# Kernel tuning notes

Measured on AMD Instinct MI355X. Metric: run time of the kernel, lower is better.

Reference implementation:

```python
import jax, jax.numpy as jnp
import numpy as np

E, N, HID, NH = 250000, 50000, 128, 4
HD = HID // NH  # head_dim = 32


def setup_inputs() -> dict:
    key = jax.random.key(0)
    ks = jax.random.split(key, 16)
    f = lambda k, s: jax.random.normal(k, s, dtype=jnp.float32)
    w = lambda k, s: jax.random.normal(k, s, dtype=jnp.float32) * 0.05
    return {
        "edge_attr": f(ks[0], (E, HID)),
        "node_features": f(ks[1], (N, HID)),
        "regime_probs": jax.random.uniform(ks[2], (3,), dtype=jnp.float32),
        # phase_query / phase_key: Linear(hidden+3 -> hidden)
        "Wq": w(ks[3], (HID, HID + 3)), "bq": jnp.zeros((HID,), jnp.float32),
        "Wk": w(ks[4], (HID, HID + 3)), "bk": jnp.zeros((HID,), jnp.float32),
        # phase_value: Linear(hidden -> hidden)
        "Wv": w(ks[5], (HID, HID)), "bv": jnp.zeros((HID,), jnp.float32),
        # nn.MultiheadAttention packed in-projection [3*hid, hid] and out_proj
        "W_in": w(ks[6], (3 * HID, HID)), "b_in": jnp.zeros((3 * HID,), jnp.float32),
        "W_mo": w(ks[7], (HID, HID)), "b_mo": jnp.zeros((HID,), jnp.float32),
        # output_proj
        "Wo": w(ks[8], (HID, HID)), "bo": jnp.zeros((HID,), jnp.float32),
        "edge_index": jax.random.randint(ks[9], (2, E), 0, N, dtype=jnp.int64),
    }


def reference(edge_attr, node_features, regime_probs,
              Wq, bq, Wk, bk, Wv, bv,
              W_in, b_in, W_mo, b_mo, Wo, bo,
              edge_index):
    e = edge_attr.shape[0]
    src = node_features[edge_index[0]]  # [E, HID] gather
    tgt = node_features[edge_index[1]]  # [E, HID] gather
    reg = jnp.broadcast_to(regime_probs, (e, regime_probs.shape[0]))  # [E, 3]

    q = jnp.concatenate([src, reg], axis=1) @ Wq.T + bq  # [E, HID]
    k = jnp.concatenate([tgt, reg], axis=1) @ Wk.T + bk  # [E, HID]
    v = edge_attr @ Wv.T + bv                             # [E, HID]

    # nn.MultiheadAttention with seq_len 1 (batch_first): in-proj, heads, softmax, out-proj
    Wiq, Wik, Wiv = jnp.split(W_in, 3, axis=0)
    biq, bik, biv = jnp.split(b_in, 3)
    q2 = (q @ Wiq.T + biq).reshape(e, NH, HD)
    k2 = (k @ Wik.T + bik).reshape(e, NH, HD)
    v2 = (v @ Wiv.T + biv).reshape(e, NH, HD)

    scale = 1.0 / jnp.sqrt(jnp.float32(HD))
    scores = jnp.sum(q2 * k2, axis=-1, keepdims=True) * scale  # [E, NH, 1]
    probs = jax.nn.softmax(scores, axis=-1)                    # seq-len-1 -> all ones
    att = (probs * v2).reshape(e, HID)                         # == v2 merged
    att = att @ W_mo.T + b_mo                                  # MHA out_proj

    out = att @ Wo.T + bo                                      # output_proj
    return edge_attr + 0.5 * out
```

## Files before the change

kernel.cpp:

```cpp
#include <hip/hip_runtime.h>
#include <hip/hip_bf16.h>

#define HID 128

typedef __attribute__((ext_vector_type(8))) short short8;
typedef __attribute__((ext_vector_type(4))) float f32x4;

static __device__ __forceinline__ short f2bf(float x) {
    __hip_bfloat16 h = __float2bfloat16(x);
    return *reinterpret_cast<short*>(&h);
}

__global__ void prep_products(const float* __restrict__ Wo,
                              const float* __restrict__ W_mo,
                              const float* __restrict__ Wiv,
                              const float* __restrict__ Wv,
                              const float* __restrict__ bv,
                              const float* __restrict__ biv,
                              const float* __restrict__ b_mo,
                              const float* __restrict__ bo,
                              float* __restrict__ Pl,
                              float* __restrict__ Pr,
                              float* __restrict__ cv)
{
    const int j = threadIdx.x;
    const int b = blockIdx.x;
    __shared__ float sh[HID];

    if (b < 256) {
        const float* A = (b < 128) ? Wo   : Wiv;
        const float* B = (b < 128) ? W_mo : Wv;
        float*       C = (b < 128) ? Pl   : Pr;
        const int i = b & 127;
        sh[j] = A[i * HID + j];
        __syncthreads();
        float s = 0.f;
        #pragma unroll 16
        for (int k = 0; k < HID; ++k) s += sh[k] * B[k * HID + j];
        C[i * HID + j] = s;
    } else {
        sh[j] = bv[j];
        __syncthreads();
        float t = biv[j];
        #pragma unroll 16
        for (int k = 0; k < HID; ++k) t += Wiv[j * HID + k] * sh[k];
        __syncthreads(); sh[j] = t; __syncthreads();
        t = b_mo[j];
        #pragma unroll 16
        for (int k = 0; k < HID; ++k) t += W_mo[j * HID + k] * sh[k];
        __syncthreads(); sh[j] = t; __syncthreads();
        t = bo[j];
        #pragma unroll 16
        for (int k = 0; k < HID; ++k) t += Wo[j * HID + k] * sh[k];
        cv[j] = 0.5f * t;
    }
}

__global__ void prep_final(const float* __restrict__ Pl,
                           const float* __restrict__ Pr,
                           __hip_bfloat16* __restrict__ Mb)
{
    const int i = blockIdx.x, j = threadIdx.x;
    __shared__ float sh[HID];
    sh[j] = Pl[i * HID + j];
    __syncthreads();
    float s = 0.f;
    #pragma unroll 16
    for (int k = 0; k < HID; ++k) s += sh[k] * Pr[k * HID + j];
    Mb[i * HID + j] = __float2bfloat16(((i == j) ? 1.0f : 0.0f) + 0.5f * s);
}

__global__ __launch_bounds__(256) void edge_gemm(
    const float* __restrict__ ea,
    const __hip_bfloat16* __restrict__ Mb,
    const float* __restrict__ cvec,
    float* __restrict__ out,
    int E, int numTiles)
{
    __shared__ __align__(16) float lds[2][2048];

    const int lane  = threadIdx.x & 63;
    const int wv    = threadIdx.x >> 6;
    const int q     = lane >> 4;
    const int c     = lane & 15;
    const int ncol0 = wv * 32;

    short8 Mfrag[2][4];
    #pragma unroll
    for (int nt = 0; nt < 2; ++nt) {
        const __hip_bfloat16* mp = Mb + (size_t)(ncol0 + nt * 16 + c) * HID + q * 8;
        #pragma unroll
        for (int kk = 0; kk < 4; ++kk)
            Mfrag[nt][kk] = *reinterpret_cast<const short8*>(mp + kk * 32);
    }
    f32x4 cvp[2];
    #pragma unroll
    for (int nt = 0; nt < 2; ++nt)
        cvp[nt] = *reinterpret_cast<const f32x4*>(cvec + ncol0 + nt * 16 + q * 4);

    int t = blockIdx.x;
    if (t >= numTiles) return;
    const int G = gridDim.x;

    const int ldrow = threadIdx.x >> 4;
    const int ldoff = (threadIdx.x & 15) * 32;
    const int wsw  = (ldrow & 7) << 4;
    const int wad0 = ldrow * 512 + (ldoff ^ wsw);
    const int wad1 = wad0 ^ 16;

    const int swz   = (c & 7) << 4;
    const int rbase = c * 512 + ((q * 32) ^ (swz & 0x60));
    const int hx    = swz & 16;

    auto load_tile = [&](int tt, float4& r0, float4& r1) {
        int row = tt * 16 + ldrow; if (row > E - 1) row = E - 1;
        const char* p = (const char*)ea + (size_t)row * 512 + ldoff;
        r0 = *reinterpret_cast<const float4*>(p);
        r1 = *reinterpret_cast<const float4*>(p + 16);
    };
    auto write_tile = [&](int buf, const float4& r0, const float4& r1) {
        char* lb = (char*)&lds[buf][0];
        *reinterpret_cast<float4*>(lb + wad0) = r0;
        *reinterpret_cast<float4*>(lb + wad1) = r1;
    };
    auto sync = [&]() {
        __builtin_amdgcn_sched_barrier(0);
        asm volatile("s_waitcnt lgkmcnt(0)" ::: "memory");
        __builtin_amdgcn_s_barrier();
        __builtin_amdgcn_sched_barrier(0);
    };
    auto compute_store = [&](int buf, int tt) {
        const char* lb = (const char*)&lds[buf][0];
        f32x4 acc[2] = { cvp[0], cvp[1] };
        #pragma unroll
        for (int kk = 0; kk < 4; ++kk) {
            const float4 f0 = *reinterpret_cast<const float4*>(lb + rbase + kk * 128 + hx);
            const float4 f1 = *reinterpret_cast<const float4*>(lb + rbase + kk * 128 + (16 ^ hx));
            short8 v;
            v[0] = f2bf(f0.x); v[1] = f2bf(f0.y); v[2] = f2bf(f0.z); v[3] = f2bf(f0.w);
            v[4] = f2bf(f1.x); v[5] = f2bf(f1.y); v[6] = f2bf(f1.z); v[7] = f2bf(f1.w);
            acc[0] = __builtin_amdgcn_mfma_f32_16x16x32_bf16(Mfrag[0][kk], v, acc[0], 0, 0, 0);
            acc[1] = __builtin_amdgcn_mfma_f32_16x16x32_bf16(Mfrag[1][kk], v, acc[1], 0, 0, 0);
        }
        const int orow = tt * 16 + c;
        if (orow < E) {
            float* op = out + (size_t)orow * HID + ncol0 + q * 4;
            *reinterpret_cast<f32x4*>(op)      = acc[0];
            *reinterpret_cast<f32x4*>(op + 16) = acc[1];
        }
    };

    float4 a0, a1, b0, b1;
    load_tile(t, a0, a1);
    bool hB = (t + G < numTiles);
    if (hB) load_tile(t + G, b0, b1);

    while (true) {
        write_tile(0, a0, a1);
        if (t + 2 * G < numTiles) load_tile(t + 2 * G, a0, a1);
        sync();
        compute_store(0, t);
        if (!hB) break;

        write_tile(1, b0, b1);
        if (t + 3 * G < numTiles) load_tile(t + 3 * G, b0, b1);
        sync();
        compute_store(1, t + G);

        t += 2 * G;
        if (t >= numTiles) break;
        hB = (t + G < numTiles);
    }
}

extern "C" void kernel_launch(void* const* d_in, const int* in_sizes, int n_in,
                              void* d_out, int out_size, void* d_ws, size_t ws_size,
                              hipStream_t stream) {
    const float* Wv   = (const float*)d_in[7];
    const float* bv   = (const float*)d_in[8];
    const float* W_in = (const float*)d_in[9];
    const float* b_in = (const float*)d_in[10];
    const float* W_mo = (const float*)d_in[11];
    const float* b_mo = (const float*)d_in[12];
    const float* Wo   = (const float*)d_in[13];
    const float* bo   = (const float*)d_in[14];
    const float* Wiv  = W_in + 2 * HID * HID;
    const float* biv  = b_in + 2 * HID;

    char* ws = (char*)d_ws;
    float*          Pl = (float*)(ws);
    float*          Pr = (float*)(ws + 65536);
    __hip_bfloat16* Mb = (__hip_bfloat16*)(ws + 131072);
    float*          cv = (float*)(ws + 163840);

    const int E = in_sizes[0] / HID;
    const int numTiles = (E + 15) / 16;
    const int grid = numTiles < 2048 ? numTiles : 2048;

    prep_products<<<dim3(257), dim3(HID), 0, stream>>>(
        Wo, W_mo, Wiv, Wv, bv, biv, b_mo, bo, Pl, Pr, cv);
    prep_final<<<dim3(HID), dim3(HID), 0, stream>>>(Pl, Pr, Mb);

    edge_gemm<<<dim3(grid), dim3(256), 0, stream>>>(
        (const float*)d_in[0], Mb, cv, (float*)d_out, E, numTiles);
}
```

Measured before the change: 278.7 us.

## Replace persistent double-buffered edge GEMM with one tile per block

```diff
diff --git a/kernel.cpp b/kernel.cpp
--- a/kernel.cpp
+++ b/kernel.cpp
@@ -77,13 +77,27 @@
     float* __restrict__ out,
     int E, int numTiles)
 {
-    __shared__ __align__(16) float lds[2][2048];
+    __shared__ __align__(16) float lds[2048];
+
+    const int t = blockIdx.x;
+    if (t >= numTiles) return;
 
     const int lane  = threadIdx.x & 63;
     const int wv    = threadIdx.x >> 6;
     const int q     = lane >> 4;
     const int c     = lane & 15;
     const int ncol0 = wv * 32;
+
+    const int ldrow = threadIdx.x >> 4;
+    const int ldoff = (threadIdx.x & 15) * 32;
+
+    float4 r0, r1;
+    {
+        int row = t * 16 + ldrow; if (row > E - 1) row = E - 1;
+        const char* p = (const char*)ea + (size_t)row * 512 + ldoff;
+        r0 = *reinterpret_cast<const float4*>(p);
+        r1 = *reinterpret_cast<const float4*>(p + 16);
+    }
 
     short8 Mfrag[2][4];
     #pragma unroll
@@ -98,78 +112,38 @@
     for (int nt = 0; nt < 2; ++nt)
         cvp[nt] = *reinterpret_cast<const f32x4*>(cvec + ncol0 + nt * 16 + q * 4);
 
-    int t = blockIdx.x;
-    if (t >= numTiles) return;
-    const int G = gridDim.x;
-
-    const int ldrow = threadIdx.x >> 4;
-    const int ldoff = (threadIdx.x & 15) * 32;
     const int wsw  = (ldrow & 7) << 4;
     const int wad0 = ldrow * 512 + (ldoff ^ wsw);
     const int wad1 = wad0 ^ 16;
+    {
+        char* lb = (char*)lds;
+        *reinterpret_cast<float4*>(lb + wad0) = r0;
+        *reinterpret_cast<float4*>(lb + wad1) = r1;
+    }
+    __syncthreads();
 
     const int swz   = (c & 7) << 4;
     const int rbase = c * 512 + ((q * 32) ^ (swz & 0x60));
     const int hx    = swz & 16;
 
-    auto load_tile = [&](int tt, float4& r0, float4& r1) {
-        int row = tt * 16 + ldrow; if (row > E - 1) row = E - 1;
-        const char* p = (const char*)ea + (size_t)row * 512 + ldoff;
-        r0 = *reinterpret_cast<const float4*>(p);
-        r1 = *reinterpret_cast<const float4*>(p + 16);
-    };
-    auto write_tile = [&](int buf, const float4& r0, const float4& r1) {
-        char* lb = (char*)&lds[buf][0];
-        *reinterpret_cast<float4*>(lb + wad0) = r0;
-        *reinterpret_cast<float4*>(lb + wad1) = r1;
-    };
-    auto sync = [&]() {
-        __builtin_amdgcn_sched_barrier(0);
-        asm volatile("s_waitcnt lgkmcnt(0)" ::: "memory");
-        __builtin_amdgcn_s_barrier();
-        __builtin_amdgcn_sched_barrier(0);
-    };
-    auto compute_store = [&](int buf, int tt) {
-        const char* lb = (const char*)&lds[buf][0];
-        f32x4 acc[2] = { cvp[0], cvp[1] };
-        #pragma unroll
-        for (int kk = 0; kk < 4; ++kk) {
-            const float4 f0 = *reinterpret_cast<const float4*>(lb + rbase + kk * 128 + hx);
-            const float4 f1 = *reinterpret_cast<const float4*>(lb + rbase + kk * 128 + (16 ^ hx));
-            short8 v;
-            v[0] = f2bf(f0.x); v[1] = f2bf(f0.y); v[2] = f2bf(f0.z); v[3] = f2bf(f0.w);
-            v[4] = f2bf(f1.x); v[5] = f2bf(f1.y); v[6] = f2bf(f1.z); v[7] = f2bf(f1.w);
-            acc[0] = __builtin_amdgcn_mfma_f32_16x16x32_bf16(Mfrag[0][kk], v, acc[0], 0, 0, 0);
-            acc[1] = __builtin_amdgcn_mfma_f32_16x16x32_bf16(Mfrag[1][kk], v, acc[1], 0, 0, 0);
-        }
-        const int orow = tt * 16 + c;
-        if (orow < E) {
-            float* op = out + (size_t)orow * HID + ncol0 + q * 4;
-            *reinterpret_cast<f32x4*>(op)      = acc[0];
-            *reinterpret_cast<f32x4*>(op + 16) = acc[1];
-        }
-    };
+    const char* lb = (const char*)lds;
+    f32x4 acc[2] = { cvp[0], cvp[1] };
+    #pragma unroll
+    for (int kk = 0; kk < 4; ++kk) {
+        const float4 f0 = *reinterpret_cast<const float4*>(lb + rbase + kk * 128 + hx);
+        const float4 f1 = *reinterpret_cast<const float4*>(lb + rbase + kk * 128 + (16 ^ hx));
+        short8 v;
+        v[0] = f2bf(f0.x); v[1] = f2bf(f0.y); v[2] = f2bf(f0.z); v[3] = f2bf(f0.w);
+        v[4] = f2bf(f1.x); v[5] = f2bf(f1.y); v[6] = f2bf(f1.z); v[7] = f2bf(f1.w);
+        acc[0] = __builtin_amdgcn_mfma_f32_16x16x32_bf16(Mfrag[0][kk], v, acc[0], 0, 0, 0);
+        acc[1] = __builtin_amdgcn_mfma_f32_16x16x32_bf16(Mfrag[1][kk], v, acc[1], 0, 0, 0);
+    }
 
-    float4 a0, a1, b0, b1;
-    load_tile(t, a0, a1);
-    bool hB = (t + G < numTiles);
-    if (hB) load_tile(t + G, b0, b1);
-
-    while (true) {
-        write_tile(0, a0, a1);
-        if (t + 2 * G < numTiles) load_tile(t + 2 * G, a0, a1);
-        sync();
-        compute_store(0, t);
-        if (!hB) break;
-
-        write_tile(1, b0, b1);
-        if (t + 3 * G < numTiles) load_tile(t + 3 * G, b0, b1);
-        sync();
-        compute_store(1, t + G);
-
-        t += 2 * G;
-        if (t >= numTiles) break;
-        hB = (t + G < numTiles);
+    const int orow = t * 16 + c;
+    if (orow < E) {
+        float* op = out + (size_t)orow * HID + ncol0 + q * 4;
+        *reinterpret_cast<f32x4*>(op)      = acc[0];
+        *reinterpret_cast<f32x4*>(op + 16) = acc[1];
     }
 }
 
@@ -195,12 +169,11 @@
 
     const int E = in_sizes[0] / HID;
     const int numTiles = (E + 15) / 16;
-    const int grid = numTiles < 2048 ? numTiles : 2048;
 
     prep_products<<<dim3(257), dim3(HID), 0, stream>>>(
         Wo, W_mo, Wiv, Wv, bv, biv, b_mo, bo, Pl, Pr, cv);
     prep_final<<<dim3(HID), dim3(HID), 0, stream>>>(Pl, Pr, Mb);
 
-    edge_gemm<<<dim3(grid), dim3(256), 0, stream>>>(
+    edge_gemm<<<dim3(numTiles), dim3(256), 0, stream>>>(
         (const float*)d_in[0], Mb, cv, (float*)d_out, E, numTiles);
 }
```

New measurement: 306.6 us. 10.0% more time.
